# Kernel optimization log

Hardware: AMD Instinct MI355X
Metric: run time of the kernel (lower is better)

## Reference

```python
import jax, jax.numpy as jnp
import numpy as np


def setup_inputs() -> dict:
    key = jax.random.key(0)
    k1, k2, k3 = jax.random.split(key, 3)
    B, T, J, D = 32, 1024, 128, 256  # D = 2 * input_dim
    ctx_embd = jax.random.normal(k1, (B, T, D), dtype=jnp.float32)
    query_embd = jax.random.normal(k2, (B, J, D), dtype=jnp.float32)
    # nn.Linear(6*input_dim, 1, bias=False) weight flattened: [w1 | w2 | w3], each of size D
    w = jax.random.normal(k3, (3 * D,), dtype=jnp.float32) * (1.0 / np.sqrt(3 * D))
    return {"ctx_embd": ctx_embd, "query_embd": query_embd, "w": w}


def reference(ctx_embd, query_embd, w):
    D = ctx_embd.shape[-1]
    w1, w2, w3 = w[:D], w[D:2 * D], w[2 * D:]
    # Trilinear score S[b,t,j] = ctx.w1 + query.w2 + (ctx*query).w3, decomposed
    # (algebraically identical to Linear(cat(ctx, query, ctx*query))).
    s_ctx = ctx_embd @ w1            # [B, T]
    s_qry = query_embd @ w2          # [B, J]
    s_mul = jnp.einsum('btd,bjd->btj', ctx_embd * w3, query_embd)  # [B, T, J]
    S = s_ctx[:, :, None] + s_qry[:, None, :] + s_mul              # [B, T, J]
    # Context-to-query attention
    a = jax.nn.softmax(S, axis=-1)                                 # [B, T, J]
    c2q = jnp.einsum('btj,bjd->btd', a, query_embd)                # [B, T, D]
    # Query-to-context attention
    b = jax.nn.softmax(jnp.max(S, axis=2), axis=-1)                # [B, T]
    q2c = jnp.einsum('bt,btd->bd', b, ctx_embd)[:, None, :]        # [B, 1, D] broadcast over T
    G = jnp.concatenate(
        [ctx_embd, c2q, ctx_embd * c2q, ctx_embd * q2c], axis=-1)  # [B, T, 4D]
    return G
```

## Files before the change

### kernel.cpp

```cpp
#include <hip/hip_runtime.h>

typedef float f4 __attribute__((ext_vector_type(4)));
typedef float f2 __attribute__((ext_vector_type(2)));
typedef short s8v __attribute__((ext_vector_type(8)));
typedef unsigned int u2v __attribute__((ext_vector_type(2)));
typedef unsigned int u4v __attribute__((ext_vector_type(4)));

#define B_ 32
#define T_ 1024
#define J_ 128
#define D_ 256

__device__ inline unsigned short f2bf(float x) {
    unsigned int u = __float_as_uint(x);
    u += 0x7fffu + ((u >> 16) & 1u);
    return (unsigned short)(u >> 16);
}

__device__ __forceinline__ void ldsload16(const void* g, void* l) {
    __builtin_amdgcn_global_load_lds(
        (const __attribute__((address_space(1))) void*)g,
        (__attribute__((address_space(3))) void*)l, 16, 0, 0);
}

__global__ __launch_bounds__(256) void k_pre(const float* __restrict__ q, const float* __restrict__ w,
                                             unsigned short* __restrict__ Bqh, float* __restrict__ sq,
                                             unsigned short* __restrict__ qTh) {
    __shared__ float t_[16][260];
    int b = blockIdx.x >> 3, jt = blockIdx.x & 7;
    int tid = threadIdx.x;
    const float* qb = q + (b * J_ + jt * 16) * D_;

#pragma unroll
    for (int k = 0; k < 4; k++) {
        int idx = tid + (k << 8);
        int jj = idx >> 6, d4 = idx & 63;
        f4 v = *(const f4*)(qb + jj * D_ + (d4 << 2));
        *(f4*)&t_[jj][d4 << 2] = v;
        f4 w1v = *(const f4*)(w + (d4 << 2));
        f4 w3v = *(const f4*)(w + 2 * D_ + (d4 << 2));
        u2v p;
        p[0] = (unsigned int)f2bf(w3v[0] * v[0] + w1v[0]) | ((unsigned int)f2bf(w3v[1] * v[1] + w1v[1]) << 16);
        p[1] = (unsigned int)f2bf(w3v[2] * v[2] + w1v[2]) | ((unsigned int)f2bf(w3v[3] * v[3] + w1v[3]) << 16);
        *(u2v*)(Bqh + (b * J_ + jt * 16 + jj) * D_ + (d4 << 2)) = p;
    }
    __syncthreads();

    {
        int jj = tid >> 4, dg = tid & 15;
        float p = 0.f;
#pragma unroll
        for (int i = 0; i < 16; i++) {
            int d = (dg << 4) + i;
            p += t_[jj][d] * w[D_ + d];
        }
#pragma unroll
        for (int m = 8; m >= 1; m >>= 1) p += __shfl_xor(p, m);
        if (dg == 0) sq[b * J_ + jt * 16 + jj] = p;
    }

    {
        int dd = tid;
        unsigned int pk[8];
#pragma unroll
        for (int i = 0; i < 8; i++) {
            pk[i] = (unsigned int)f2bf(t_[2 * i][dd]) | ((unsigned int)f2bf(t_[2 * i + 1][dd]) << 16);
        }
        u4v v0, v1;
        v0[0] = pk[0]; v0[1] = pk[1]; v0[2] = pk[2]; v0[3] = pk[3];
        v1[0] = pk[4]; v1[1] = pk[5]; v1[2] = pk[6]; v1[3] = pk[7];
        unsigned short* dst = qTh + (b * D_ + dd) * J_ + jt * 16;
        *(u4v*)dst = v0;
        *(u4v*)(dst + 8) = v1;
    }
}

__global__ __launch_bounds__(256, 4) void k_main(const float* __restrict__ ctx,
                                                 const unsigned short* __restrict__ Bqh,
                                                 const unsigned short* __restrict__ qTh,
                                                 const float* __restrict__ sq,
                                                 float* __restrict__ pq2c, float* __restrict__ pms,
                                                 float* __restrict__ out) {
    __shared__ __align__(16) char lds[40960];
    char* B0 = lds;
    char* B1 = lds + 16384;
    char* Ps = lds + 32768;
    float* sc = (float*)B1;

    int bid = blockIdx.x;
    int b  = ((bid & 7) << 2) | ((bid >> 3) & 3);
    int tc = bid >> 5;
    int t0 = tc << 5;
    int tid = threadIdx.x;
    int w = tid >> 6, l = tid & 63, lr = l & 15, lq = l >> 4;
    int rg = w & 1, ch = w >> 1;
    int R0 = rg << 4;

    const unsigned short* BqB  = Bqh + b * J_ * D_;
    const unsigned short* qThB = qTh + b * D_ * J_;

    auto stageBq = [&](char* buf, int qt) {
#pragma unroll
        for (int i = 0; i < 4; i++) {
            int g = tid + (i << 8);
            int jr = g >> 3, c = g & 7;
            ldsload16(BqB + jr * D_ + (qt << 6) + ((c ^ (jr & 7)) << 3),
                      buf + (i << 12) + (w << 10));
        }
    };
    auto stageQ = [&](char* buf, int st) {
#pragma unroll
        for (int i = 0; i < 4; i++) {
            int g = tid + (i << 8);
            int dr = g >> 4, c = g & 15;
            ldsload16(qThB + ((st << 6) + dr) * J_ + ((c ^ (dr & 7)) << 3),
                      buf + (i << 12) + (w << 10));
        }
    };

    f4 acc[4];
#pragma unroll
    for (int nf = 0; nf < 4; nf++) acc[nf] = (f4){0.f, 0.f, 0.f, 0.f};

    stageBq(B0, 0);
    stageBq(B1, 1);

    const float* ctxA = ctx + (b * T_ + t0 + R0 + lr) * D_;
    s8v af[8];
#pragma unroll
    for (int k = 0; k < 8; k++) {
        f4 a0 = *(const f4*)(ctxA + k * 32 + lq * 8);
        f4 a1 = *(const f4*)(ctxA + k * 32 + lq * 8 + 4);
        union { unsigned short u[8]; s8v v; } t;
#pragma unroll
        for (int e = 0; e < 4; e++) { t.u[e] = f2bf(a0[e]); t.u[e + 4] = f2bf(a1[e]); }
        af[k] = t.v;
    }

    auto mfmaA = [&](char* buf, int qt) {
#pragma unroll
        for (int kk = 0; kk < 2; kk++)
#pragma unroll
            for (int nf = 0; nf < 4; nf++) {
                int jr = (ch << 6) + (nf << 4) + lr;
                s8v bv = *(const s8v*)(buf + (jr << 7) + ((((kk << 2) | lq) ^ (jr & 7)) << 4));
                acc[nf] = __builtin_amdgcn_mfma_f32_16x16x32_bf16(af[(qt << 1) | kk], bv, acc[nf], 0, 0, 0);
            }
    };

    __syncthreads();
    mfmaA(B0, 0);
    __syncthreads();
    stageBq(B0, 2);
    mfmaA(B1, 1);
    __syncthreads();
    stageBq(B1, 3);
    mfmaA(B0, 2);
    __syncthreads();
    stageQ(B0, 0);
    mfmaA(B1, 3);

    float sqv[4];
#pragma unroll
    for (int nf = 0; nf < 4; nf++) sqv[nf] = sq[b * J_ + (ch << 6) + (nf << 4) + lr];
    float mp[4], sp[4];
#pragma unroll
    for (int r = 0; r < 4; r++) {
        float m = -1e30f;
#pragma unroll
        for (int nf = 0; nf < 4; nf++) { acc[nf][r] += sqv[nf]; m = fmaxf(m, acc[nf][r]); }
#pragma unroll
        for (int msk = 8; msk >= 1; msk >>= 1) m = fmaxf(m, __shfl_xor(m, msk));
        float s = 0.f;
#pragma unroll
        for (int nf = 0; nf < 4; nf++) { float e = __expf(acc[nf][r] - m); acc[nf][r] = e; s += e; }
#pragma unroll
        for (int msk = 8; msk >= 1; msk >>= 1) s += __shfl_xor(s, msk);
        mp[r] = m; sp[r] = s;
    }
    __syncthreads();
    if (lr == 0) {
#pragma unroll
        for (int r = 0; r < 4; r++) {
            int row = R0 + (lq << 2) + r;
            sc[(row << 2) + (ch << 1)] = mp[r];
            sc[(row << 2) + (ch << 1) + 1] = sp[r];
        }
    }
    __syncthreads();

    float mm[4];
#pragma unroll
    for (int r = 0; r < 4; r++) {
        int row = R0 + (lq << 2) + r;
        float m0 = sc[(row << 2)],     s0 = sc[(row << 2) + 1];
        float m1 = sc[(row << 2) + 2], s1 = sc[(row << 2) + 3];
        float m = fmaxf(m0, m1);
        float sum = s0 * __expf(m0 - m) + s1 * __expf(m1 - m);
        float scale = __expf(mp[r] - m) / sum;
#pragma unroll
        for (int nf = 0; nf < 4; nf++) {
            int cc = (ch << 6) + (nf << 4) + lr;
            int chunk = cc >> 3;
            *(unsigned short*)(Ps + row * 256 + ((chunk ^ (row & 7)) << 4) + ((lr & 7) << 1)) =
                f2bf(acc[nf][r] * scale);
        }
        mm[r] = m;
    }
    __syncthreads();
    stageQ(B1, 1);

    int prow = R0 + lr;
    s8v pf[4];
#pragma unroll
    for (int jk = 0; jk < 4; jk++)
        pf[jk] = *(const s8v*)(Ps + prow * 256 + ((((jk << 2) + lq) ^ (prow & 7)) << 4));

    f4 acc2[8];
#pragma unroll
    for (int ai = 0; ai < 8; ai++) acc2[ai] = (f4){0.f, 0.f, 0.f, 0.f};

    auto mfmaB = [&](char* rb, int s) {
#pragma unroll
        for (int df2 = 0; df2 < 2; df2++) {
            int dr = (ch << 5) + (df2 << 4) + lr;
            int ai = (s << 1) + df2;
#pragma unroll
            for (int jk = 0; jk < 4; jk++) {
                s8v bv = *(const s8v*)(rb + (dr << 8) + ((((jk << 2) + lq) ^ (dr & 7)) << 4));
                acc2[ai] = __builtin_amdgcn_mfma_f32_16x16x32_bf16(pf[jk], bv, acc2[ai], 0, 0, 0);
            }
        }
    };

    mfmaB(B0, 0);
    __syncthreads();
    stageQ(B0, 2);
    mfmaB(B1, 1);
    __syncthreads();
    stageQ(B1, 3);
    mfmaB(B0, 2);
    __syncthreads();
    mfmaB(B1, 3);
    __syncthreads();

    float* cq = (float*)lds;
#pragma unroll
    for (int s2 = 0; s2 < 4; s2++)
#pragma unroll
        for (int df2 = 0; df2 < 2; df2++) {
            int col = (s2 << 6) + (ch << 5) + (df2 << 4) + lr;
            int ai = (s2 << 1) + df2;
            int chunk = col >> 2;
#pragma unroll
            for (int r = 0; r < 4; r++) {
                int row = R0 + (lq << 2) + r;
                *(float*)((char*)cq + (row << 10) + ((chunk ^ (row & 7)) << 4) + ((col & 3) << 2)) = acc2[ai][r];
            }
        }
    __syncthreads();

    {
        int row = tid >> 3;
        int o = b * T_ + t0 + row;
        const float* crow = ctx + o * D_;
        float* orow = out + o * 1024;
#pragma unroll
        for (int i = 0; i < 8; i++) {
            int col4 = (i << 5) + ((tid & 7) << 2);
            int chunk = col4 >> 2;
            f4 val = *(const f4*)((char*)cq + (row << 10) + ((chunk ^ (row & 7)) << 4));
            f4 cx = *(const f4*)(crow + col4);
            f4 v3 = cx * val;
            __builtin_nontemporal_store(cx, (f4*)(orow + col4));
            __builtin_nontemporal_store(val, (f4*)(orow + 256 + col4));
            __builtin_nontemporal_store(v3, (f4*)(orow + 512 + col4));
        }
    }

    {
        float m16[16];
#pragma unroll
        for (int i = 0; i < 16; i++) m16[i] = __shfl(mm[i & 3], (i >> 2) << 4);
        float mw = -1e30f;
#pragma unroll
        for (int i = 0; i < 16; i++) mw = fmaxf(mw, m16[i]);
        const float* cp = ctx + (b * T_ + t0 + R0) * D_ + (ch << 7) + (l << 1);
        f2 p = (f2){0.f, 0.f};
        float sw_ = 0.f;
#pragma unroll 4
        for (int t = 0; t < 16; t++) {
            float e = __expf(m16[t] - mw);
            sw_ += e;
            f2 cv = *(const f2*)(cp + t * D_);
            p.x += e * cv.x; p.y += e * cv.y;
        }
        int pidx = (((b << 5) | tc) << 1) | rg;
        *(f2*)(pq2c + (pidx << 8) + (ch << 7) + (l << 1)) = p;
        if (ch == 0 && l == 0) { pms[pidx * 2] = mw; pms[pidx * 2 + 1] = sw_; }
    }
}

__global__ __launch_bounds__(256) void k_tail(const float* __restrict__ ctx,
                                              const float* __restrict__ pq2c, const float* __restrict__ pms,
                                              float* __restrict__ out) {
    int b = blockIdx.x >> 5, tc = blockIdx.x & 31;
    int tid = threadIdx.x;
    const float* pm = pms + b * 128;

    float mx = -1e30f;
#pragma unroll 8
    for (int i = 0; i < 64; i++) mx = fmaxf(mx, pm[2 * i]);
    float sm = 0.f, q2 = 0.f;
#pragma unroll 4
    for (int i = 0; i < 64; i++) {
        float e = __expf(pm[2 * i] - mx);
        sm += pm[2 * i + 1] * e;
        q2 += e * pq2c[((b << 6) + i) * 256 + tid];
    }
    q2 /= sm;
    __shared__ float q2s[256];
    q2s[tid] = q2;
    __syncthreads();

    int row = tid >> 3;
    int o = b * T_ + tc * 32 + row;
    const float* crow = ctx + o * D_;
    float* orow = out + o * 1024;
#pragma unroll
    for (int i = 0; i < 8; i++) {
        int col4 = (i << 5) + ((tid & 7) << 2);
        f4 cx = *(const f4*)(crow + col4);
        f4 qv = *(const f4*)&q2s[col4];
        f4 r = cx * qv;
        __builtin_nontemporal_store(r, (f4*)(orow + 768 + col4));
    }
}

extern "C" void kernel_launch(void* const* d_in, const int* in_sizes, int n_in,
                              void* d_out, int out_size, void* d_ws, size_t ws_size,
                              hipStream_t stream) {
    const float* ctx   = (const float*)d_in[0];
    const float* query = (const float*)d_in[1];
    const float* w     = (const float*)d_in[2];
    float* out = (float*)d_out;

    unsigned short* Bqh = (unsigned short*)d_ws;
    unsigned short* qTh = Bqh + B_ * J_ * D_;
    float* fws = (float*)(qTh + B_ * J_ * D_);
    float* sq   = fws;
    float* pq2c = fws + 4096;
    float* pms  = fws + 4096 + 2048 * 256;

    k_pre<<<B_ * 8, 256, 0, stream>>>(query, w, Bqh, sq, qTh);
    k_main<<<B_ * (T_ / 32), 256, 0, stream>>>(ctx, Bqh, qTh, sq, pq2c, pms, out);
    k_tail<<<B_ * 32, 256, 0, stream>>>(ctx, pq2c, pms, out);
}
```

Before: 66.74 us.

## Shrink LDS staging buffers and deepen pipeline to raise k_main occupancy

Halves the size of each LDS stage buffer: K-chunks for the score GEMM go from 64 to 32, and the c2q GEMM goes from 64 to 32 d-rows. Each phase therefore becomes an 8-step double-buffered pipeline instead of 4. The c2q tile is written back through LDS in two 16-row halves, so LDS use drops from 40KB to about 25KB and launch bounds rise to 6 blocks per CU. Block-to-batch mapping switches from a swizzled order to a linear one, and the sq load is hoisted. The trade-off is more barriers and smaller per-stage transfers, in exchange for higher occupancy and better latency hiding.

```diff
diff --git a/kernel.cpp b/kernel.cpp
--- a/kernel.cpp
+++ b/kernel.cpp
@@ -75,21 +75,21 @@
     }
 }
 
-__global__ __launch_bounds__(256, 4) void k_main(const float* __restrict__ ctx,
+__global__ __launch_bounds__(256, 6) void k_main(const float* __restrict__ ctx,
                                                  const unsigned short* __restrict__ Bqh,
                                                  const unsigned short* __restrict__ qTh,
                                                  const float* __restrict__ sq,
                                                  float* __restrict__ pq2c, float* __restrict__ pms,
                                                  float* __restrict__ out) {
-    __shared__ __align__(16) char lds[40960];
+    __shared__ __align__(16) char lds[25088];
     char* B0 = lds;
-    char* B1 = lds + 16384;
-    char* Ps = lds + 32768;
-    float* sc = (float*)B1;
+    char* B1 = lds + 8192;
+    char* Ps = lds + 16384;
+    float* sc = (float*)(lds + 24576);
 
     int bid = blockIdx.x;
-    int b  = ((bid & 7) << 2) | ((bid >> 3) & 3);
-    int tc = bid >> 5;
+    int b  = bid >> 5;
+    int tc = bid & 31;
     int t0 = tc << 5;
     int tid = threadIdx.x;
     int w = tid >> 6, l = tid & 63, lr = l & 15, lq = l >> 4;
@@ -99,22 +99,22 @@
     const unsigned short* BqB  = Bqh + b * J_ * D_;
     const unsigned short* qThB = qTh + b * D_ * J_;
 
-    auto stageBq = [&](char* buf, int qt) {
-#pragma unroll
-        for (int i = 0; i < 4; i++) {
+    auto stageA = [&](char* buf, int sa) {
+#pragma unroll
+        for (int i = 0; i < 2; i++) {
             int g = tid + (i << 8);
-            int jr = g >> 3, c = g & 7;
-            ldsload16(BqB + jr * D_ + (qt << 6) + ((c ^ (jr & 7)) << 3),
-                      buf + (i << 12) + (w << 10));
+            int line = g >> 3, s8 = g & 7;
+            int L = s8 ^ (line & 7);
+            int jr = (line << 1) | (L >> 2);
+            ldsload16(BqB + jr * D_ + sa * 32 + ((L & 3) << 3), buf + (g << 4));
         }
     };
-    auto stageQ = [&](char* buf, int st) {
-#pragma unroll
-        for (int i = 0; i < 4; i++) {
+    auto stageQ = [&](char* buf, int sb) {
+#pragma unroll
+        for (int i = 0; i < 2; i++) {
             int g = tid + (i << 8);
             int dr = g >> 4, c = g & 15;
-            ldsload16(qThB + ((st << 6) + dr) * J_ + ((c ^ (dr & 7)) << 3),
-                      buf + (i << 12) + (w << 10));
+            ldsload16(qThB + (sb * 32 + dr) * J_ + ((c ^ (dr & 7)) << 3), buf + (g << 4));
         }
     };
 
@@ -122,8 +122,12 @@
 #pragma unroll
     for (int nf = 0; nf < 4; nf++) acc[nf] = (f4){0.f, 0.f, 0.f, 0.f};
 
-    stageBq(B0, 0);
-    stageBq(B1, 1);
+    stageA(B0, 0);
+    stageA(B1, 1);
+
+    float sqv[4];
+#pragma unroll
+    for (int nf = 0; nf < 4; nf++) sqv[nf] = sq[b * J_ + (ch << 6) + (nf << 4) + lr];
 
     const float* ctxA = ctx + (b * T_ + t0 + R0 + lr) * D_;
     s8v af[8];
@@ -137,32 +141,27 @@
         af[k] = t.v;
     }
 
-    auto mfmaA = [&](char* buf, int qt) {
-#pragma unroll
-        for (int kk = 0; kk < 2; kk++)
-#pragma unroll
-            for (int nf = 0; nf < 4; nf++) {
-                int jr = (ch << 6) + (nf << 4) + lr;
-                s8v bv = *(const s8v*)(buf + (jr << 7) + ((((kk << 2) | lq) ^ (jr & 7)) << 4));
-                acc[nf] = __builtin_amdgcn_mfma_f32_16x16x32_bf16(af[(qt << 1) | kk], bv, acc[nf], 0, 0, 0);
-            }
+    auto mfmaA = [&](char* buf, int sa) {
+#pragma unroll
+        for (int nf = 0; nf < 4; nf++) {
+            int jr = (ch << 6) + (nf << 4) + lr;
+            int line = jr >> 1;
+            int slot = (((jr & 1) << 2) | lq) ^ (line & 7);
+            s8v bv = *(const s8v*)(buf + (line << 7) + (slot << 4));
+            acc[nf] = __builtin_amdgcn_mfma_f32_16x16x32_bf16(af[sa], bv, acc[nf], 0, 0, 0);
+        }
     };
 
     __syncthreads();
     mfmaA(B0, 0);
-    __syncthreads();
-    stageBq(B0, 2);
-    mfmaA(B1, 1);
-    __syncthreads();
-    stageBq(B1, 3);
-    mfmaA(B0, 2);
-    __syncthreads();
-    stageQ(B0, 0);
-    mfmaA(B1, 3);
-
-    float sqv[4];
-#pragma unroll
-    for (int nf = 0; nf < 4; nf++) sqv[nf] = sq[b * J_ + (ch << 6) + (nf << 4) + lr];
+    __syncthreads(); stageA(B0, 2); mfmaA(B1, 1);
+    __syncthreads(); stageA(B1, 3); mfmaA(B0, 2);
+    __syncthreads(); stageA(B0, 4); mfmaA(B1, 3);
+    __syncthreads(); stageA(B1, 5); mfmaA(B0, 4);
+    __syncthreads(); stageA(B0, 6); mfmaA(B1, 5);
+    __syncthreads(); stageA(B1, 7); mfmaA(B0, 6);
+    __syncthreads(); mfmaA(B1, 7);
+
     float mp[4], sp[4];
 #pragma unroll
     for (int r = 0; r < 4; r++) {
@@ -178,7 +177,6 @@
         for (int msk = 8; msk >= 1; msk >>= 1) s += __shfl_xor(s, msk);
         mp[r] = m; sp[r] = s;
     }
-    __syncthreads();
     if (lr == 0) {
 #pragma unroll
         for (int r = 0; r < 4; r++) {
@@ -188,6 +186,8 @@
         }
     }
     __syncthreads();
+    stageQ(B0, 0);
+    stageQ(B1, 1);
 
     float mm[4];
 #pragma unroll
@@ -208,7 +208,6 @@
         mm[r] = m;
     }
     __syncthreads();
-    stageQ(B1, 1);
 
     int prow = R0 + lr;
     s8v pf[4];
@@ -220,62 +219,59 @@
 #pragma unroll
     for (int ai = 0; ai < 8; ai++) acc2[ai] = (f4){0.f, 0.f, 0.f, 0.f};
 
-    auto mfmaB = [&](char* rb, int s) {
-#pragma unroll
-        for (int df2 = 0; df2 < 2; df2++) {
-            int dr = (ch << 5) + (df2 << 4) + lr;
-            int ai = (s << 1) + df2;
-#pragma unroll
-            for (int jk = 0; jk < 4; jk++) {
-                s8v bv = *(const s8v*)(rb + (dr << 8) + ((((jk << 2) + lq) ^ (dr & 7)) << 4));
-                acc2[ai] = __builtin_amdgcn_mfma_f32_16x16x32_bf16(pf[jk], bv, acc2[ai], 0, 0, 0);
+    int drB = (ch << 4) + lr;
+    auto mfmaB = [&](char* rb, int sb) {
+#pragma unroll
+        for (int jk = 0; jk < 4; jk++) {
+            s8v bv = *(const s8v*)(rb + (drB << 8) + ((((jk << 2) | lq) ^ (drB & 7)) << 4));
+            acc2[sb] = __builtin_amdgcn_mfma_f32_16x16x32_bf16(pf[jk], bv, acc2[sb], 0, 0, 0);
+        }
+    };
+
+    mfmaB(B0, 0);
+    __syncthreads(); stageQ(B0, 2); mfmaB(B1, 1);
+    __syncthreads(); stageQ(B1, 3); mfmaB(B0, 2);
+    __syncthreads(); stageQ(B0, 4); mfmaB(B1, 3);
+    __syncthreads(); stageQ(B1, 5); mfmaB(B0, 4);
+    __syncthreads(); stageQ(B0, 6); mfmaB(B1, 5);
+    __syncthreads(); stageQ(B1, 7); mfmaB(B0, 6);
+    __syncthreads(); mfmaB(B1, 7);
+    __syncthreads();
+
+    float* cq = (float*)lds;
+#pragma unroll
+    for (int p = 0; p < 2; p++) {
+        if (rg == p) {
+#pragma unroll
+            for (int sb = 0; sb < 8; sb++) {
+                int col = (sb << 5) + (ch << 4) + lr;
+                int chunk = col >> 2;
+#pragma unroll
+                for (int r = 0; r < 4; r++) {
+                    int lrow = (lq << 2) + r;
+                    *(float*)((char*)cq + (lrow << 10) + ((chunk ^ (lrow & 7)) << 4) + ((col & 3) << 2)) = acc2[sb][r];
+                }
             }
         }
-    };
-
-    mfmaB(B0, 0);
-    __syncthreads();
-    stageQ(B0, 2);
-    mfmaB(B1, 1);
-    __syncthreads();
-    stageQ(B1, 3);
-    mfmaB(B0, 2);
-    __syncthreads();
-    mfmaB(B1, 3);
-    __syncthreads();
-
-    float* cq = (float*)lds;
-#pragma unroll
-    for (int s2 = 0; s2 < 4; s2++)
-#pragma unroll
-        for (int df2 = 0; df2 < 2; df2++) {
-            int col = (s2 << 6) + (ch << 5) + (df2 << 4) + lr;
-            int ai = (s2 << 1) + df2;
-            int chunk = col >> 2;
-#pragma unroll
-            for (int r = 0; r < 4; r++) {
-                int row = R0 + (lq << 2) + r;
-                *(float*)((char*)cq + (row << 10) + ((chunk ^ (row & 7)) << 4) + ((col & 3) << 2)) = acc2[ai][r];
+        __syncthreads();
+        {
+            int lrow = tid >> 4;
+            int o = b * T_ + t0 + (p << 4) + lrow;
+            const float* crow = ctx + o * D_;
+            float* orow = out + o * 1024;
+#pragma unroll
+            for (int i = 0; i < 4; i++) {
+                int col4 = (i << 6) + ((tid & 15) << 2);
+                int chunk = col4 >> 2;
+                f4 val = *(const f4*)((char*)cq + (lrow << 10) + ((chunk ^ (lrow & 7)) << 4));
+                f4 cx = *(const f4*)(crow + col4);
+                f4 v3 = cx * val;
+                __builtin_nontemporal_store(cx, (f4*)(orow + col4));
+                __builtin_nontemporal_store(val, (f4*)(orow + 256 + col4));
+                __builtin_nontemporal_store(v3, (f4*)(orow + 512 + col4));
             }
         }
-    __syncthreads();
-
-    {
-        int row = tid >> 3;
-        int o = b * T_ + t0 + row;
-        const float* crow = ctx + o * D_;
-        float* orow = out + o * 1024;
-#pragma unroll
-        for (int i = 0; i < 8; i++) {
-            int col4 = (i << 5) + ((tid & 7) << 2);
-            int chunk = col4 >> 2;
-            f4 val = *(const f4*)((char*)cq + (row << 10) + ((chunk ^ (row & 7)) << 4));
-            f4 cx = *(const f4*)(crow + col4);
-            f4 v3 = cx * val;
-            __builtin_nontemporal_store(cx, (f4*)(orow + col4));
-            __builtin_nontemporal_store(val, (f4*)(orow + 256 + col4));
-            __builtin_nontemporal_store(v3, (f4*)(orow + 512 + col4));
-        }
+        __syncthreads();
     }
 
     {
@@ -295,7 +291,7 @@
             f2 cv = *(const f2*)(cp + t * D_);
             p.x += e * cv.x; p.y += e * cv.y;
         }
-        int pidx = (((b << 5) | tc) << 1) | rg;
+        int pidx = (bid << 1) | rg;
         *(f2*)(pq2c + (pidx << 8) + (ch << 7) + (l << 1)) = p;
         if (ch == 0 && l == 0) { pms[pidx * 2] = mw; pms[pidx * 2 + 1] = sw_; }
     }
```

New measurement: 77.03 us. 15.4% more time.

## Process 64 context rows per block to reuse staged query tiles

Applied to the files above, without the earlier changes.

Each k_main block now handles two 32-row groups of context. Every staged B/query tile in LDS feeds twice as many MFMAs, and the grid is halved. The cost is doubled accumulator and fragment register state, so launch bounds drop to 3 blocks per CU, with fewer blocks in flight and more register pressure. The epilogue and q2c partials are run per 32-row group to keep the partial layout the same.

```diff
diff --git a/kernel.cpp b/kernel.cpp
--- a/kernel.cpp
+++ b/kernel.cpp
@@ -75,7 +75,7 @@
     }
 }
 
-__global__ __launch_bounds__(256, 4) void k_main(const float* __restrict__ ctx,
+__global__ __launch_bounds__(256, 3) void k_main(const float* __restrict__ ctx,
                                                  const unsigned short* __restrict__ Bqh,
                                                  const unsigned short* __restrict__ qTh,
                                                  const float* __restrict__ sq,
@@ -86,11 +86,12 @@
     char* B1 = lds + 16384;
     char* Ps = lds + 32768;
     float* sc = (float*)B1;
+    char* PB = B1 + 1024;
 
     int bid = blockIdx.x;
     int b  = ((bid & 7) << 2) | ((bid >> 3) & 3);
-    int tc = bid >> 5;
-    int t0 = tc << 5;
+    int tt = bid >> 5;
+    int t0 = tt << 6;
     int tid = threadIdx.x;
     int w = tid >> 6, l = tid & 63, lr = l & 15, lq = l >> 4;
     int rg = w & 1, ch = w >> 1;
@@ -118,109 +119,156 @@
         }
     };
 
-    f4 acc[4];
-#pragma unroll
-    for (int nf = 0; nf < 4; nf++) acc[nf] = (f4){0.f, 0.f, 0.f, 0.f};
+    f4 acc0[4], acc1[4];
+#pragma unroll
+    for (int nf = 0; nf < 4; nf++) { acc0[nf] = (f4){0.f,0.f,0.f,0.f}; acc1[nf] = (f4){0.f,0.f,0.f,0.f}; }
 
     stageBq(B0, 0);
     stageBq(B1, 1);
 
-    const float* ctxA = ctx + (b * T_ + t0 + R0 + lr) * D_;
-    s8v af[8];
+    const float* ctxA0 = ctx + (b * T_ + t0 + R0 + lr) * D_;
+    const float* ctxA1 = ctxA0 + 32 * D_;
+    s8v af0[8], af1[8];
 #pragma unroll
     for (int k = 0; k < 8; k++) {
-        f4 a0 = *(const f4*)(ctxA + k * 32 + lq * 8);
-        f4 a1 = *(const f4*)(ctxA + k * 32 + lq * 8 + 4);
+        f4 a0 = *(const f4*)(ctxA0 + k * 32 + lq * 8);
+        f4 a1 = *(const f4*)(ctxA0 + k * 32 + lq * 8 + 4);
         union { unsigned short u[8]; s8v v; } t;
 #pragma unroll
         for (int e = 0; e < 4; e++) { t.u[e] = f2bf(a0[e]); t.u[e + 4] = f2bf(a1[e]); }
-        af[k] = t.v;
-    }
-
-    auto mfmaA = [&](char* buf, int qt) {
+        af0[k] = t.v;
+    }
+#pragma unroll
+    for (int k = 0; k < 8; k++) {
+        f4 a0 = *(const f4*)(ctxA1 + k * 32 + lq * 8);
+        f4 a1 = *(const f4*)(ctxA1 + k * 32 + lq * 8 + 4);
+        union { unsigned short u[8]; s8v v; } t;
+#pragma unroll
+        for (int e = 0; e < 4; e++) { t.u[e] = f2bf(a0[e]); t.u[e + 4] = f2bf(a1[e]); }
+        af1[k] = t.v;
+    }
+
+    auto mfmaA2 = [&](char* buf, int qt) {
 #pragma unroll
         for (int kk = 0; kk < 2; kk++)
 #pragma unroll
             for (int nf = 0; nf < 4; nf++) {
                 int jr = (ch << 6) + (nf << 4) + lr;
                 s8v bv = *(const s8v*)(buf + (jr << 7) + ((((kk << 2) | lq) ^ (jr & 7)) << 4));
-                acc[nf] = __builtin_amdgcn_mfma_f32_16x16x32_bf16(af[(qt << 1) | kk], bv, acc[nf], 0, 0, 0);
+                acc0[nf] = __builtin_amdgcn_mfma_f32_16x16x32_bf16(af0[(qt << 1) | kk], bv, acc0[nf], 0, 0, 0);
+                acc1[nf] = __builtin_amdgcn_mfma_f32_16x16x32_bf16(af1[(qt << 1) | kk], bv, acc1[nf], 0, 0, 0);
             }
     };
 
     __syncthreads();
-    mfmaA(B0, 0);
+    mfmaA2(B0, 0);
     __syncthreads();
     stageBq(B0, 2);
-    mfmaA(B1, 1);
+    mfmaA2(B1, 1);
     __syncthreads();
     stageBq(B1, 3);
-    mfmaA(B0, 2);
+    mfmaA2(B0, 2);
     __syncthreads();
     stageQ(B0, 0);
-    mfmaA(B1, 3);
+    mfmaA2(B1, 3);
 
     float sqv[4];
 #pragma unroll
     for (int nf = 0; nf < 4; nf++) sqv[nf] = sq[b * J_ + (ch << 6) + (nf << 4) + lr];
-    float mp[4], sp[4];
+    float mp0[4], sp0[4], mp1[4], sp1[4];
 #pragma unroll
     for (int r = 0; r < 4; r++) {
         float m = -1e30f;
 #pragma unroll
-        for (int nf = 0; nf < 4; nf++) { acc[nf][r] += sqv[nf]; m = fmaxf(m, acc[nf][r]); }
+        for (int nf = 0; nf < 4; nf++) { acc0[nf][r] += sqv[nf]; m = fmaxf(m, acc0[nf][r]); }
 #pragma unroll
         for (int msk = 8; msk >= 1; msk >>= 1) m = fmaxf(m, __shfl_xor(m, msk));
         float s = 0.f;
 #pragma unroll
-        for (int nf = 0; nf < 4; nf++) { float e = __expf(acc[nf][r] - m); acc[nf][r] = e; s += e; }
+        for (int nf = 0; nf < 4; nf++) { float e = __expf(acc0[nf][r] - m); acc0[nf][r] = e; s += e; }
 #pragma unroll
         for (int msk = 8; msk >= 1; msk >>= 1) s += __shfl_xor(s, msk);
-        mp[r] = m; sp[r] = s;
+        mp0[r] = m; sp0[r] = s;
+    }
+#pragma unroll
+    for (int r = 0; r < 4; r++) {
+        float m = -1e30f;
+#pragma unroll
+        for (int nf = 0; nf < 4; nf++) { acc1[nf][r] += sqv[nf]; m = fmaxf(m, acc1[nf][r]); }
+#pragma unroll
+        for (int msk = 8; msk >= 1; msk >>= 1) m = fmaxf(m, __shfl_xor(m, msk));
+        float s = 0.f;
+#pragma unroll
+        for (int nf = 0; nf < 4; nf++) { float e = __expf(acc1[nf][r] - m); acc1[nf][r] = e; s += e; }
+#pragma unroll
+        for (int msk = 8; msk >= 1; msk >>= 1) s += __shfl_xor(s, msk);
+        mp1[r] = m; sp1[r] = s;
     }
     __syncthreads();
     if (lr == 0) {
 #pragma unroll
         for (int r = 0; r < 4; r++) {
             int row = R0 + (lq << 2) + r;
-            sc[(row << 2) + (ch << 1)] = mp[r];
-            sc[(row << 2) + (ch << 1) + 1] = sp[r];
-        }
-    }
-    __syncthreads();
-
-    float mm[4];
+            sc[(row << 2) + (ch << 1)] = mp0[r];
+            sc[(row << 2) + (ch << 1) + 1] = sp0[r];
+            sc[((32 + row) << 2) + (ch << 1)] = mp1[r];
+            sc[((32 + row) << 2) + (ch << 1) + 1] = sp1[r];
+        }
+    }
+    __syncthreads();
+
+    float mm0[4], mm1[4];
 #pragma unroll
     for (int r = 0; r < 4; r++) {
         int row = R0 + (lq << 2) + r;
         float m0 = sc[(row << 2)],     s0 = sc[(row << 2) + 1];
-        float m1 = sc[(row << 2) + 2], s1 = sc[(row << 2) + 3];
-        float m = fmaxf(m0, m1);
-        float sum = s0 * __expf(m0 - m) + s1 * __expf(m1 - m);
-        float scale = __expf(mp[r] - m) / sum;
+        float m1v = sc[(row << 2) + 2], s1v = sc[(row << 2) + 3];
+        float m = fmaxf(m0, m1v);
+        float sum = s0 * __expf(m0 - m) + s1v * __expf(m1v - m);
+        float scale = __expf(mp0[r] - m) / sum;
 #pragma unroll
         for (int nf = 0; nf < 4; nf++) {
             int cc = (ch << 6) + (nf << 4) + lr;
             int chunk = cc >> 3;
             *(unsigned short*)(Ps + row * 256 + ((chunk ^ (row & 7)) << 4) + ((lr & 7) << 1)) =
-                f2bf(acc[nf][r] * scale);
-        }
-        mm[r] = m;
+                f2bf(acc0[nf][r] * scale);
+        }
+        mm0[r] = m;
+    }
+#pragma unroll
+    for (int r = 0; r < 4; r++) {
+        int row = R0 + (lq << 2) + r;
+        float m0 = sc[((32 + row) << 2)],     s0 = sc[((32 + row) << 2) + 1];
+        float m1v = sc[((32 + row) << 2) + 2], s1v = sc[((32 + row) << 2) + 3];
+        float m = fmaxf(m0, m1v);
+        float sum = s0 * __expf(m0 - m) + s1v * __expf(m1v - m);
+        float scale = __expf(mp1[r] - m) / sum;
+#pragma unroll
+        for (int nf = 0; nf < 4; nf++) {
+            int cc = (ch << 6) + (nf << 4) + lr;
+            int chunk = cc >> 3;
+            *(unsigned short*)(PB + row * 256 + ((chunk ^ (row & 7)) << 4) + ((lr & 7) << 1)) =
+                f2bf(acc1[nf][r] * scale);
+        }
+        mm1[r] = m;
+    }
+    __syncthreads();
+
+    int prow = R0 + lr;
+    s8v pf0[4], pf1[4];
+#pragma unroll
+    for (int jk = 0; jk < 4; jk++) {
+        pf0[jk] = *(const s8v*)(Ps + prow * 256 + ((((jk << 2) + lq) ^ (prow & 7)) << 4));
+        pf1[jk] = *(const s8v*)(PB + prow * 256 + ((((jk << 2) + lq) ^ (prow & 7)) << 4));
     }
     __syncthreads();
     stageQ(B1, 1);
 
-    int prow = R0 + lr;
-    s8v pf[4];
-#pragma unroll
-    for (int jk = 0; jk < 4; jk++)
-        pf[jk] = *(const s8v*)(Ps + prow * 256 + ((((jk << 2) + lq) ^ (prow & 7)) << 4));
-
-    f4 acc2[8];
-#pragma unroll
-    for (int ai = 0; ai < 8; ai++) acc2[ai] = (f4){0.f, 0.f, 0.f, 0.f};
-
-    auto mfmaB = [&](char* rb, int s) {
+    f4 accB0[8], accB1[8];
+#pragma unroll
+    for (int ai = 0; ai < 8; ai++) { accB0[ai] = (f4){0.f,0.f,0.f,0.f}; accB1[ai] = (f4){0.f,0.f,0.f,0.f}; }
+
+    auto mfmaB2 = [&](char* rb, int s) {
 #pragma unroll
         for (int df2 = 0; df2 < 2; df2++) {
             int dr = (ch << 5) + (df2 << 4) + lr;
@@ -228,41 +276,41 @@
 #pragma unroll
             for (int jk = 0; jk < 4; jk++) {
                 s8v bv = *(const s8v*)(rb + (dr << 8) + ((((jk << 2) + lq) ^ (dr & 7)) << 4));
-                acc2[ai] = __builtin_amdgcn_mfma_f32_16x16x32_bf16(pf[jk], bv, acc2[ai], 0, 0, 0);
+                accB0[ai] = __builtin_amdgcn_mfma_f32_16x16x32_bf16(pf0[jk], bv, accB0[ai], 0, 0, 0);
+                accB1[ai] = __builtin_amdgcn_mfma_f32_16x16x32_bf16(pf1[jk], bv, accB1[ai], 0, 0, 0);
             }
         }
     };
 
-    mfmaB(B0, 0);
+    mfmaB2(B0, 0);
     __syncthreads();
     stageQ(B0, 2);
-    mfmaB(B1, 1);
+    mfmaB2(B1, 1);
     __syncthreads();
     stageQ(B1, 3);
-    mfmaB(B0, 2);
-    __syncthreads();
-    mfmaB(B1, 3);
-    __syncthreads();
-
-    float* cq = (float*)lds;
-#pragma unroll
-    for (int s2 = 0; s2 < 4; s2++)
-#pragma unroll
-        for (int df2 = 0; df2 < 2; df2++) {
-            int col = (s2 << 6) + (ch << 5) + (df2 << 4) + lr;
-            int ai = (s2 << 1) + df2;
-            int chunk = col >> 2;
-#pragma unroll
-            for (int r = 0; r < 4; r++) {
-                int row = R0 + (lq << 2) + r;
-                *(float*)((char*)cq + (row << 10) + ((chunk ^ (row & 7)) << 4) + ((col & 3) << 2)) = acc2[ai][r];
+    mfmaB2(B0, 2);
+    __syncthreads();
+    mfmaB2(B1, 3);
+    __syncthreads();
+
+    auto epiPass = [&](const f4 (&A)[8], int p) {
+        float* cq = (float*)lds;
+#pragma unroll
+        for (int s2 = 0; s2 < 4; s2++)
+#pragma unroll
+            for (int df2 = 0; df2 < 2; df2++) {
+                int col = (s2 << 6) + (ch << 5) + (df2 << 4) + lr;
+                int ai = (s2 << 1) + df2;
+                int chunk = col >> 2;
+#pragma unroll
+                for (int r = 0; r < 4; r++) {
+                    int row = R0 + (lq << 2) + r;
+                    *(float*)((char*)cq + (row << 10) + ((chunk ^ (row & 7)) << 4) + ((col & 3) << 2)) = A[ai][r];
+                }
             }
-        }
-    __syncthreads();
-
-    {
+        __syncthreads();
         int row = tid >> 3;
-        int o = b * T_ + t0 + row;
+        int o = b * T_ + t0 + (p << 5) + row;
         const float* crow = ctx + o * D_;
         float* orow = out + o * 1024;
 #pragma unroll
@@ -276,16 +324,19 @@
             __builtin_nontemporal_store(val, (f4*)(orow + 256 + col4));
             __builtin_nontemporal_store(v3, (f4*)(orow + 512 + col4));
         }
-    }
-
-    {
+    };
+    epiPass(accB0, 0);
+    __syncthreads();
+    epiPass(accB1, 1);
+
+    auto q2cPart = [&](const float (&mmg)[4], int g) {
         float m16[16];
 #pragma unroll
-        for (int i = 0; i < 16; i++) m16[i] = __shfl(mm[i & 3], (i >> 2) << 4);
+        for (int i = 0; i < 16; i++) m16[i] = __shfl(mmg[i & 3], (i >> 2) << 4);
         float mw = -1e30f;
 #pragma unroll
         for (int i = 0; i < 16; i++) mw = fmaxf(mw, m16[i]);
-        const float* cp = ctx + (b * T_ + t0 + R0) * D_ + (ch << 7) + (l << 1);
+        const float* cp = ctx + (b * T_ + t0 + (g << 5) + R0) * D_ + (ch << 7) + (l << 1);
         f2 p = (f2){0.f, 0.f};
         float sw_ = 0.f;
 #pragma unroll 4
@@ -295,10 +346,13 @@
             f2 cv = *(const f2*)(cp + t * D_);
             p.x += e * cv.x; p.y += e * cv.y;
         }
-        int pidx = (((b << 5) | tc) << 1) | rg;
+        int tc32 = (tt << 1) | g;
+        int pidx = (((b << 5) | tc32) << 1) | rg;
         *(f2*)(pq2c + (pidx << 8) + (ch << 7) + (l << 1)) = p;
         if (ch == 0 && l == 0) { pms[pidx * 2] = mw; pms[pidx * 2 + 1] = sw_; }
-    }
+    };
+    q2cPart(mm0, 0);
+    q2cPart(mm1, 1);
 }
 
 __global__ __launch_bounds__(256) void k_tail(const float* __restrict__ ctx,
@@ -353,6 +407,6 @@
     float* pms  = fws + 4096 + 2048 * 256;
 
     k_pre<<<B_ * 8, 256, 0, stream>>>(query, w, Bqh, sq, qTh);
-    k_main<<<B_ * (T_ / 32), 256, 0, stream>>>(ctx, Bqh, qTh, sq, pq2c, pms, out);
+    k_main<<<B_ * (T_ / 64), 256, 0, stream>>>(ctx, Bqh, qTh, sq, pq2c, pms, out);
     k_tail<<<B_ * 32, 256, 0, stream>>>(ctx, pq2c, pms, out);
 }
```

Result: slower. 73.51 us (+10.1%).

## Read MFMA B operands directly from global instead of LDS double-buffering

Applied to the files above, without the earlier changes.

Drops the global_load_lds staging of the query operand tiles (Bq and qT) into double-buffered LDS and reads the MFMA B fragments straight from global memory (L2/L1 cached). This cuts LDS from 40KB to 32KB and removes most barriers, and the launch bound is raised to 5 blocks per CU to improve occupancy. The risk is more global and cache traffic with less latency hiding, since each wave now issues uncoalesced 16-byte loads per MFMA.

```diff
diff --git a/kernel.cpp b/kernel.cpp
--- a/kernel.cpp
+++ b/kernel.cpp
@@ -15,12 +15,6 @@
     unsigned int u = __float_as_uint(x);
     u += 0x7fffu + ((u >> 16) & 1u);
     return (unsigned short)(u >> 16);
-}
-
-__device__ __forceinline__ void ldsload16(const void* g, void* l) {
-    __builtin_amdgcn_global_load_lds(
-        (const __attribute__((address_space(1))) void*)g,
-        (__attribute__((address_space(3))) void*)l, 16, 0, 0);
 }
 
 __global__ __launch_bounds__(256) void k_pre(const float* __restrict__ q, const float* __restrict__ w,
@@ -75,17 +69,15 @@
     }
 }
 
-__global__ __launch_bounds__(256, 4) void k_main(const float* __restrict__ ctx,
+__global__ __launch_bounds__(256, 5) void k_main(const float* __restrict__ ctx,
                                                  const unsigned short* __restrict__ Bqh,
                                                  const unsigned short* __restrict__ qTh,
                                                  const float* __restrict__ sq,
                                                  float* __restrict__ pq2c, float* __restrict__ pms,
                                                  float* __restrict__ out) {
-    __shared__ __align__(16) char lds[40960];
-    char* B0 = lds;
-    char* B1 = lds + 16384;
-    char* Ps = lds + 32768;
-    float* sc = (float*)B1;
+    __shared__ __align__(16) char lds[32768];
+    char* Ps = lds;
+    float* sc = (float*)(lds + 8192);
 
     int bid = blockIdx.x;
     int b  = ((bid & 7) << 2) | ((bid >> 3) & 3);
@@ -99,32 +91,6 @@
     const unsigned short* BqB  = Bqh + b * J_ * D_;
     const unsigned short* qThB = qTh + b * D_ * J_;
 
-    auto stageBq = [&](char* buf, int qt) {
-#pragma unroll
-        for (int i = 0; i < 4; i++) {
-            int g = tid + (i << 8);
-            int jr = g >> 3, c = g & 7;
-            ldsload16(BqB + jr * D_ + (qt << 6) + ((c ^ (jr & 7)) << 3),
-                      buf + (i << 12) + (w << 10));
-        }
-    };
-    auto stageQ = [&](char* buf, int st) {
-#pragma unroll
-        for (int i = 0; i < 4; i++) {
-            int g = tid + (i << 8);
-            int dr = g >> 4, c = g & 15;
-            ldsload16(qThB + ((st << 6) + dr) * J_ + ((c ^ (dr & 7)) << 3),
-                      buf + (i << 12) + (w << 10));
-        }
-    };
-
-    f4 acc[4];
-#pragma unroll
-    for (int nf = 0; nf < 4; nf++) acc[nf] = (f4){0.f, 0.f, 0.f, 0.f};
-
-    stageBq(B0, 0);
-    stageBq(B1, 1);
-
     const float* ctxA = ctx + (b * T_ + t0 + R0 + lr) * D_;
     s8v af[8];
 #pragma unroll
@@ -137,33 +103,24 @@
         af[k] = t.v;
     }
 
-    auto mfmaA = [&](char* buf, int qt) {
-#pragma unroll
-        for (int kk = 0; kk < 2; kk++)
-#pragma unroll
-            for (int nf = 0; nf < 4; nf++) {
-                int jr = (ch << 6) + (nf << 4) + lr;
-                s8v bv = *(const s8v*)(buf + (jr << 7) + ((((kk << 2) | lq) ^ (jr & 7)) << 4));
-                acc[nf] = __builtin_amdgcn_mfma_f32_16x16x32_bf16(af[(qt << 1) | kk], bv, acc[nf], 0, 0, 0);
-            }
-    };
-
-    __syncthreads();
-    mfmaA(B0, 0);
-    __syncthreads();
-    stageBq(B0, 2);
-    mfmaA(B1, 1);
-    __syncthreads();
-    stageBq(B1, 3);
-    mfmaA(B0, 2);
-    __syncthreads();
-    stageQ(B0, 0);
-    mfmaA(B1, 3);
+    f4 acc[4];
+#pragma unroll
+    for (int nf = 0; nf < 4; nf++) acc[nf] = (f4){0.f, 0.f, 0.f, 0.f};
+
+#pragma unroll
+    for (int k = 0; k < 8; k++) {
+#pragma unroll
+        for (int nf = 0; nf < 4; nf++) {
+            int jr = (ch << 6) + (nf << 4) + lr;
+            s8v bv = *(const s8v*)(BqB + jr * D_ + (k << 5) + (lq << 3));
+            acc[nf] = __builtin_amdgcn_mfma_f32_16x16x32_bf16(af[k], bv, acc[nf], 0, 0, 0);
+        }
+    }
 
     float sqv[4];
 #pragma unroll
     for (int nf = 0; nf < 4; nf++) sqv[nf] = sq[b * J_ + (ch << 6) + (nf << 4) + lr];
-    float mp[4], sp[4];
+    float mp[4];
 #pragma unroll
     for (int r = 0; r < 4; r++) {
         float m = -1e30f;
@@ -176,15 +133,11 @@
         for (int nf = 0; nf < 4; nf++) { float e = __expf(acc[nf][r] - m); acc[nf][r] = e; s += e; }
 #pragma unroll
         for (int msk = 8; msk >= 1; msk >>= 1) s += __shfl_xor(s, msk);
-        mp[r] = m; sp[r] = s;
-    }
-    __syncthreads();
-    if (lr == 0) {
-#pragma unroll
-        for (int r = 0; r < 4; r++) {
+        mp[r] = m;
+        if (lr == 0) {
             int row = R0 + (lq << 2) + r;
-            sc[(row << 2) + (ch << 1)] = mp[r];
-            sc[(row << 2) + (ch << 1) + 1] = sp[r];
+            sc[(row << 2) + (ch << 1)] = m;
+            sc[(row << 2) + (ch << 1) + 1] = s;
         }
     }
     __syncthreads();
@@ -208,41 +161,30 @@
         mm[r] = m;
     }
     __syncthreads();
-    stageQ(B1, 1);
 
     int prow = R0 + lr;
     s8v pf[4];
 #pragma unroll
     for (int jk = 0; jk < 4; jk++)
         pf[jk] = *(const s8v*)(Ps + prow * 256 + ((((jk << 2) + lq) ^ (prow & 7)) << 4));
+    __syncthreads();
 
     f4 acc2[8];
 #pragma unroll
     for (int ai = 0; ai < 8; ai++) acc2[ai] = (f4){0.f, 0.f, 0.f, 0.f};
 
-    auto mfmaB = [&](char* rb, int s) {
+#pragma unroll
+    for (int st = 0; st < 4; st++)
 #pragma unroll
         for (int df2 = 0; df2 < 2; df2++) {
-            int dr = (ch << 5) + (df2 << 4) + lr;
-            int ai = (s << 1) + df2;
+            int dr = (st << 6) + (ch << 5) + (df2 << 4) + lr;
+            int ai = (st << 1) + df2;
 #pragma unroll
             for (int jk = 0; jk < 4; jk++) {
-                s8v bv = *(const s8v*)(rb + (dr << 8) + ((((jk << 2) + lq) ^ (dr & 7)) << 4));
+                s8v bv = *(const s8v*)(qThB + dr * J_ + (jk << 5) + (lq << 3));
                 acc2[ai] = __builtin_amdgcn_mfma_f32_16x16x32_bf16(pf[jk], bv, acc2[ai], 0, 0, 0);
             }
         }
-    };
-
-    mfmaB(B0, 0);
-    __syncthreads();
-    stageQ(B0, 2);
-    mfmaB(B1, 1);
-    __syncthreads();
-    stageQ(B1, 3);
-    mfmaB(B0, 2);
-    __syncthreads();
-    mfmaB(B1, 3);
-    __syncthreads();
 
     float* cq = (float*)lds;
 #pragma unroll
```

Result: slower. 85.66 us (+28.4%).
